# Kernel tuning notes

Measured on AMD Instinct MI355X. Metric: run time of the kernel, lower is better.

The kernel has to match this reference:

```python
import math
import jax, jax.numpy as jnp
import numpy as np

B, C, H, W = 8, 128, 128, 128

def _cosine_basis(n):
    pos = (jnp.arange(n, dtype=jnp.float32) + 0.5) / n          # [n]
    freq = jnp.arange(n, dtype=jnp.float32)[:, None]            # [n,1]
    basis = jnp.cos(freq * pos[None, :] * math.pi) * math.sqrt(2.0 / n)
    return basis.at[0, :].multiply(1.0 / math.sqrt(2.0))        # [n,n]


def setup_inputs() -> dict:
    key = jax.random.key(0)
    ks = jax.random.split(key, 12)
    s = 0.02
    return {
        "x":        jax.random.normal(ks[0], (B, C, H, W), jnp.float32),
        "dw_w":     jax.random.normal(ks[1], (C, 1, 3, 3), jnp.float32) * s,
        "dw_b":     jnp.zeros((C,), jnp.float32),
        "in_w":     jax.random.normal(ks[2], (2 * C, C), jnp.float32) * s,
        "in_b":     jnp.zeros((2 * C,), jnp.float32),
        "out_w":    jax.random.normal(ks[3], (C, C), jnp.float32) * s,
        "out_b":    jnp.zeros((C,), jnp.float32),
        "ln_w":     jnp.ones((C,), jnp.float32),
        "ln_b":     jnp.zeros((C,), jnp.float32),
        "ph_w":     jax.random.normal(ks[4], (C, C), jnp.float32) * s,
        "ph_b":     jnp.zeros((C,), jnp.float32),
        "wave_speed": jnp.ones((1,), jnp.float32),
        "damping":    jnp.full((1,), 0.1, jnp.float32),
        "freq_embed": jax.random.normal(ks[5], (H, W, C), jnp.float32) * s,
    }


def reference(x, dw_w, dw_b, in_w, in_b, out_w, out_b, ln_w, ln_b,
              ph_w, ph_b, wave_speed, damping, freq_embed):
    # depthwise 3x3 conv (groups=C), padding=1
    mixed = jax.lax.conv_general_dilated(
        x, dw_w, window_strides=(1, 1), padding=((1, 1), (1, 1)),
        dimension_numbers=("NCHW", "OIHW", "NCHW"), feature_group_count=C)
    mixed = mixed + dw_b[None, :, None, None]
    mixed = jnp.transpose(mixed, (0, 2, 3, 1))                  # [B,H,W,C]

    proj = mixed @ in_w.T + in_b                                # [B,H,W,2C]
    carrier, gate = jnp.split(proj, 2, axis=-1)

    cos_h = _cosine_basis(H)
    cos_w = _cosine_basis(W)
    # DCT-II along H then W
    spectral = jnp.einsum("bhwc,nh->bnwc", carrier, cos_h)
    spectral = jnp.einsum("bnwc,mw->bnmc", spectral, cos_w)     # [B,H,W,C] (freq)

    # phase modulation (base_resolution == H == W, so no resize)
    phase = jax.nn.gelu(freq_embed @ ph_w.T + ph_b, approximate=False)  # [H,W,C]
    wave_phase = wave_speed * phase                             # broadcast [H,W,C]
    vel_scale = jnp.sin(wave_phase) / jnp.maximum(jnp.abs(wave_speed), 1e-6)
    modulated = (jnp.cos(wave_phase) + vel_scale * (1.0 + 0.5 * damping)) * spectral

    # inverse DCT
    fused = jnp.einsum("bnmc,wm->bnwc", modulated, cos_w.T)
    fused = jnp.einsum("bnwc,hn->bhwc", fused, cos_h.T)         # [B,H,W,C]

    # LayerNorm over channels
    mu = jnp.mean(fused, axis=-1, keepdims=True)
    var = jnp.mean(jnp.square(fused - mu), axis=-1, keepdims=True)
    fused = (fused - mu) / jnp.sqrt(var + 1e-5) * ln_w + ln_b

    fused = fused * jax.nn.silu(gate)
    out = fused @ out_w.T + out_b                               # [B,H,W,C]
    return jnp.transpose(out, (0, 3, 1, 2))                     # [B,C,H,W]
```

## Files before the change

kernel.cpp:

```cpp
#include <hip/hip_runtime.h>
#include <math.h>

#ifndef M_PI
#define M_PI 3.14159265358979323846
#endif

typedef float fx4 __attribute__((ext_vector_type(4)));
typedef __bf16 bf16x8 __attribute__((ext_vector_type(8)));
typedef __bf16 bf16x4 __attribute__((ext_vector_type(4)));

__device__ __forceinline__ unsigned short f2bf(float f){
  union { float f; unsigned u; } v; v.f = f;
  unsigned r = v.u + 0x7FFFu + ((v.u >> 16) & 1u);
  return (unsigned short)(r >> 16);
}
__device__ __forceinline__ float bf2f(unsigned short u){
  union { unsigned u; float f; } v; v.u = ((unsigned)u) << 16;
  return v.f;
}
__device__ __forceinline__ int swz(int row, int colbyte){
  return row*256 + (colbyte ^ ((row & 7) << 4));
}

template<typename FA, typename FB>
__device__ __forceinline__ void run_gemm(FA la, FB lb, fx4 (&acc)[4][4]){
  bf16x8 a[2][4], b[2][4];
  #pragma unroll
  for (int mi=0;mi<4;mi++){ a[0][mi]=la(mi,0); b[0][mi]=lb(mi,0); }
  #pragma unroll
  for (int ks=0; ks<4; ks++){
    int cur = ks&1, nxt = cur^1;
    if (ks<3){
      #pragma unroll
      for (int mi=0;mi<4;mi++){ a[nxt][mi]=la(mi,ks+1); b[nxt][mi]=lb(mi,ks+1); }
    }
    #pragma unroll
    for (int mi=0;mi<4;mi++)
      #pragma unroll
      for (int ni=0;ni<4;ni++)
        acc[mi][ni] = __builtin_amdgcn_mfma_f32_16x16x32_bf16(a[cur][mi], b[cur][ni], acc[mi][ni], 0, 0, 0);
  }
}

__global__ __launch_bounds__(128) void prep_kernel(
    const float* __restrict__ in_w, const float* __restrict__ ph_w,
    const float* __restrict__ out_w,
    unsigned short* __restrict__ basis_bf, unsigned short* __restrict__ basisT_bf,
    unsigned short* __restrict__ ph_w_bf, unsigned short* __restrict__ in_w_bf,
    unsigned short* __restrict__ out_w_bf)
{
  int n = blockIdx.x;
  int h = threadIdx.x;
  double arg = (double)(n*(2*h+1)) * (M_PI/256.0);
  double v = cos(arg) * 0.125;
  if (n==0) v *= 0.7071067811865476;
  unsigned short bv = f2bf((float)v);
  basis_bf[n*128+h]  = bv;
  basisT_bf[h*128+n] = bv;
  ph_w_bf[n*128+h]  = f2bf(ph_w[n*128+h]);
  in_w_bf[n*128+h]        = f2bf(in_w[n*128+h]);
  in_w_bf[(n+128)*128+h]  = f2bf(in_w[(n+128)*128+h]);
  out_w_bf[n*128+h]       = f2bf(out_w[n*128+h]);
}

__global__ __launch_bounds__(256) void castfe_kernel(
  const float* __restrict__ fe, unsigned short* __restrict__ feb)
{
  int idx = blockIdx.x*256 + threadIdx.x;
  const float* s = fe + (size_t)idx*8;
  float4 f0 = *(const float4*)s;
  float4 f1 = *(const float4*)(s+4);
  unsigned short o[8];
  o[0]=f2bf(f0.x); o[1]=f2bf(f0.y); o[2]=f2bf(f0.z); o[3]=f2bf(f0.w);
  o[4]=f2bf(f1.x); o[5]=f2bf(f1.y); o[6]=f2bf(f1.z); o[7]=f2bf(f1.w);
  *(int4*)(feb + (size_t)idx*8) = *(const int4*)o;
}

__global__ __launch_bounds__(256) void projk_kernel(
  const unsigned short* __restrict__ feb, const unsigned short* __restrict__ ph_w_bf,
  float* __restrict__ projT)
{
  int r0 = blockIdx.x * 128;
  int t = threadIdx.x;
  int l = t & 63, wid = t >> 6;
  int wm = wid >> 1, wn = wid & 1;
  int lr = l & 15, lk = (l>>4)*8, ld4 = (l>>4)*4;
  fx4 acc[4][4];
  #pragma unroll
  for (int i=0;i<4;i++) for (int j=0;j<4;j++) acc[i][j] = (fx4){0.f,0.f,0.f,0.f};
  run_gemm(
    [&](int mi,int ks)->bf16x8{ return *(const bf16x8*)(feb + (size_t)(r0 + wm*64+mi*16+lr)*128 + ks*32+lk); },
    [&](int ni,int ks)->bf16x8{ return *(const bf16x8*)(ph_w_bf + (size_t)(wn*64+ni*16+lr)*128 + ks*32+lk); },
    acc);
  #pragma unroll
  for (int mi=0;mi<4;mi++)
    #pragma unroll
    for (int ni=0;ni<4;ni++){
      int c = wn*64 + ni*16 + lr;
      int r = r0 + wm*64 + mi*16 + ld4;
      *(fx4*)(projT + (size_t)c*16384 + r) = acc[mi][ni];
    }
}

__global__ __launch_bounds__(256) void modfin_kernel(
  const float* __restrict__ projT, const float* __restrict__ ph_b,
  const float* __restrict__ wave_speed, const float* __restrict__ damping,
  float* __restrict__ modT)
{
  int blk = blockIdx.x;
  int c = blk >> 4, qb = blk & 15;
  int t = threadIdx.x;
  int q = qb*8 + (t>>5);
  int p0 = (t & 31)*4;
  float ws0 = wave_speed[0];
  float dmp = damping[0];
  float inv = 1.0f / fmaxf(fabsf(ws0), 1e-6f);
  float dampf = 1.0f + 0.5f*dmp;
  float bc = ph_b[c];
  const float* src = projT + (size_t)c*16384 + q;
  float o[4];
  #pragma unroll
  for (int i=0;i<4;i++){
    float v = src[(size_t)(p0+i)*128] + bc;
    float g = 0.5f*v*(1.0f + erff(v*0.70710678118f));
    float wp = ws0*g;
    o[i] = __cosf(wp) + __sinf(wp)*inv*dampf;
  }
  *(float4*)(modT + ((size_t)c*128 + q)*128 + p0) = make_float4(o[0],o[1],o[2],o[3]);
}

__global__ __launch_bounds__(256) void dwconv_kernel(
  const float* __restrict__ x, const float* __restrict__ dw_w,
  const float* __restrict__ dw_b, unsigned short* __restrict__ conv)
{
  int blk = blockIdx.x;
  int plane = blk >> 2, band = blk & 3;
  int c = plane & 127;
  const float* xp = x + (size_t)plane*16384;
  unsigned short* op = conv + (size_t)plane*16384;
  const float* kw = dw_w + c*9;
  float k0=kw[0],k1=kw[1],k2=kw[2],k3=kw[3],k4=kw[4],k5=kw[5],k6=kw[6],k7=kw[7],k8=kw[8];
  float bias = dw_b[c];
  int t = threadIdx.x;
  int q = t & 31;
  int w0 = q*4;
  int rg = t >> 5;
  int h0 = band*32 + rg*4;
  bool le = (q==0), re = (q==31);

  float4 fA, fB, fC; float lA,rA,lB,rB,lC,rC;
  #define LOADROW(hh, f, l, r) { \
    int hc = (hh)<0 ? 0 : ((hh)>127 ? 127 : (hh)); \
    f = *(const float4*)(xp + hc*128 + w0); \
    float lu = __shfl_up(f.w, 1, 32); \
    float rd = __shfl_down(f.x, 1, 32); \
    l = le ? 0.f : lu; \
    r = re ? 0.f : rd; \
    if ((hh)<0 || (hh)>127){ f = make_float4(0.f,0.f,0.f,0.f); l=0.f; r=0.f; } \
  }
  LOADROW(h0-1, fA,lA,rA);
  LOADROW(h0,   fB,lB,rB);
  #pragma unroll
  for (int i=0;i<4;i++){
    LOADROW(h0+1+i, fC,lC,rC);
    float4 o;
    o.x = bias; o.y = bias; o.z = bias; o.w = bias;
    o.x = fmaf(k0,lA,  fmaf(k1,fA.x, fmaf(k2,fA.y, o.x)));
    o.y = fmaf(k0,fA.x,fmaf(k1,fA.y, fmaf(k2,fA.z, o.y)));
    o.z = fmaf(k0,fA.y,fmaf(k1,fA.z, fmaf(k2,fA.w, o.z)));
    o.w = fmaf(k0,fA.z,fmaf(k1,fA.w, fmaf(k2,rA,   o.w)));
    o.x = fmaf(k3,lB,  fmaf(k4,fB.x, fmaf(k5,fB.y, o.x)));
    o.y = fmaf(k3,fB.x,fmaf(k4,fB.y, fmaf(k5,fB.z, o.y)));
    o.z = fmaf(k3,fB.y,fmaf(k4,fB.z, fmaf(k5,fB.w, o.z)));
    o.w = fmaf(k3,fB.z,fmaf(k4,fB.w, fmaf(k5,rB,   o.w)));
    o.x = fmaf(k6,lC,  fmaf(k7,fC.x, fmaf(k8,fC.y, o.x)));
    o.y = fmaf(k6,fC.x,fmaf(k7,fC.y, fmaf(k8,fC.z, o.y)));
    o.z = fmaf(k6,fC.y,fmaf(k7,fC.z, fmaf(k8,fC.w, o.z)));
    o.w = fmaf(k6,fC.z,fmaf(k7,fC.w, fmaf(k8,rC,   o.w)));
    bf16x4 v;
    v[0]=(__bf16)o.x; v[1]=(__bf16)o.y; v[2]=(__bf16)o.z; v[3]=(__bf16)o.w;
    *(bf16x4*)(op + (size_t)(h0+i)*128 + w0) = v;
    fA=fB; lA=lB; rA=rB;
    fB=fC; lB=lC; rB=rC;
  }
  #undef LOADROW
}

__global__ __launch_bounds__(512) void inproj_kernel(
  const unsigned short* __restrict__ conv, const unsigned short* __restrict__ in_w_bf,
  const float* __restrict__ in_b, unsigned short* __restrict__ carrier,
  unsigned short* __restrict__ gate)
{
  __shared__ char A[32768];
  int blk = blockIdx.x; int b = blk>>7, h = blk&127;
  const unsigned short* C = conv + (size_t)b*2097152 + h*128;
  int t = threadIdx.x;
  {
    int wl = t & 63, grp = t >> 6;
    #pragma unroll
    for (int p=0;p<2;p++){
      int w = wl + 64*p;
      #pragma unroll
      for (int q=0;q<4;q++){
        int c0 = (q*8 + grp)*4;
        ushort4 v;
        v.x = C[(size_t)(c0+0)*16384 + w];
        v.y = C[(size_t)(c0+1)*16384 + w];
        v.z = C[(size_t)(c0+2)*16384 + w];
        v.w = C[(size_t)(c0+3)*16384 + w];
        *(ushort4*)(A + swz(w, c0*2)) = v;
      }
    }
  }
  __syncthreads();
  int l = t & 63, wid = t >> 6;
  int wm = wid >> 2, wn = wid & 3;
  int lr = l & 15, lk = (l>>4)*8, ld4 = (l>>4)*4;
  fx4 acc[4][4];
  #pragma unroll
  for (int i=0;i<4;i++) for (int j=0;j<4;j++) acc[i][j] = (fx4){0.f,0.f,0.f,0.f};
  run_gemm(
    [&](int mi,int ks)->bf16x8{ return *(const bf16x8*)(A + swz(wm*64+mi*16+lr, (ks*32+lk)*2)); },
    [&](int ni,int ks)->bf16x8{ return *(const bf16x8*)(in_w_bf + (size_t)(wn*64+ni*16+lr)*128 + ks*32+lk); },
    acc);
  __syncthreads();
  if (wn < 2){
    #pragma unroll
    for (int mi=0;mi<4;mi++)
      #pragma unroll
      for (int ni=0;ni<4;ni++){
        int n = wn*64 + ni*16 + lr;
        int w0 = wm*64 + mi*16 + ld4;
        float bias = in_b[n];
        ushort4 v;
        v.x=f2bf(acc[mi][ni][0]+bias); v.y=f2bf(acc[mi][ni][1]+bias);
        v.z=f2bf(acc[mi][ni][2]+bias); v.w=f2bf(acc[mi][ni][3]+bias);
        *(ushort4*)(carrier + (size_t)(b*128+n)*16384 + h*128 + w0) = v;
      }
  } else {
    #pragma unroll
    for (int mi=0;mi<4;mi++)
      #pragma unroll
      for (int ni=0;ni<4;ni++){
        int n = wn*64 + ni*16 + lr;
        int c = n - 128;
        int w0 = wm*64 + mi*16 + ld4;
        float bias = in_b[n];
        #pragma unroll
        for (int r=0;r<4;r++){
          float v = acc[mi][ni][r] + bias;
          float s = v / (1.0f + __expf(-v));
          *(unsigned short*)(A + swz(w0+r, c*2)) = f2bf(s);
        }
      }
  }
  __syncthreads();
  {
    unsigned short* gout = gate + (size_t)blk*16384;
    int w = t >> 2, cq = (t & 3) * 32;
    #pragma unroll
    for (int i=0;i<4;i++){
      int c0 = cq + i*8;
      int4 v = *(const int4*)(A + swz(w, c0*2));
      *(int4*)(gout + w*128 + c0) = v;
    }
  }
}

__global__ __launch_bounds__(256) void wave_kernel(
  const unsigned short* __restrict__ carrier,
  const unsigned short* __restrict__ basis,
  const unsigned short* __restrict__ basisT,
  const float* __restrict__ modT,
  unsigned short* __restrict__ fused)
{
  __shared__ char U[32768];
  int blk = blockIdx.x;
  int c = blk & 127;
  const unsigned short* X = carrier + (size_t)blk*16384;
  unsigned short* F = fused + (size_t)blk*16384;
  int t = threadIdx.x;
  int l = t & 63, wid = t >> 6;
  int wm = wid >> 1, wn = wid & 1;
  int lr = l & 15, lk = (l>>4)*8, ld4 = (l>>4)*4;
  fx4 acc[4][4];

  #pragma unroll
  for (int i=0;i<4;i++) for (int j=0;j<4;j++) acc[i][j] = (fx4){0.f,0.f,0.f,0.f};
  run_gemm(
    [&](int mi,int ks)->bf16x8{ return *(const bf16x8*)(X + (size_t)(wm*64+mi*16+lr)*128 + ks*32+lk); },
    [&](int ni,int ks)->bf16x8{ return *(const bf16x8*)(basis + (size_t)(wn*64+ni*16+lr)*128 + ks*32+lk); },
    acc);
  #pragma unroll
  for (int mi=0;mi<4;mi++)
    #pragma unroll
    for (int ni=0;ni<4;ni++){
      int m = wn*64 + ni*16 + lr, h0 = wm*64 + mi*16 + ld4;
      ushort4 v;
      v.x=f2bf(acc[mi][ni][0]); v.y=f2bf(acc[mi][ni][1]);
      v.z=f2bf(acc[mi][ni][2]); v.w=f2bf(acc[mi][ni][3]);
      *(ushort4*)(U + swz(m, h0*2)) = v;
    }
  __syncthreads();

  #pragma unroll
  for (int i=0;i<4;i++) for (int j=0;j<4;j++) acc[i][j] = (fx4){0.f,0.f,0.f,0.f};
  run_gemm(
    [&](int mi,int ks)->bf16x8{ return *(const bf16x8*)(basis + (size_t)(wm*64+mi*16+lr)*128 + ks*32+lk); },
    [&](int ni,int ks)->bf16x8{ return *(const bf16x8*)(U + swz(wn*64+ni*16+lr, (ks*32+lk)*2)); },
    acc);
  {
    const float* Mc = modT + (size_t)c*16384;
    #pragma unroll
    for (int mi=0;mi<4;mi++)
      #pragma unroll
      for (int ni=0;ni<4;ni++){
        int n0 = wm*64 + mi*16 + ld4, m = wn*64 + ni*16 + lr;
        fx4 mv = *(const fx4*)(Mc + (size_t)m*128 + n0);
        acc[mi][ni] *= mv;
      }
  }
  __syncthreads();
  #pragma unroll
  for (int mi=0;mi<4;mi++)
    #pragma unroll
    for (int ni=0;ni<4;ni++){
      int m = wn*64 + ni*16 + lr, n0 = wm*64 + mi*16 + ld4;
      ushort4 v;
      v.x=f2bf(acc[mi][ni][0]); v.y=f2bf(acc[mi][ni][1]);
      v.z=f2bf(acc[mi][ni][2]); v.w=f2bf(acc[mi][ni][3]);
      *(ushort4*)(U + swz(m, n0*2)) = v;
    }
  __syncthreads();

  #pragma unroll
  for (int i=0;i<4;i++) for (int j=0;j<4;j++) acc[i][j] = (fx4){0.f,0.f,0.f,0.f};
  run_gemm(
    [&](int mi,int ks)->bf16x8{ return *(const bf16x8*)(U + swz(wm*64+mi*16+lr, (ks*32+lk)*2)); },
    [&](int ni,int ks)->bf16x8{ return *(const bf16x8*)(basisT + (size_t)(wn*64+ni*16+lr)*128 + ks*32+lk); },
    acc);
  __syncthreads();
  #pragma unroll
  for (int mi=0;mi<4;mi++)
    #pragma unroll
    for (int ni=0;ni<4;ni++){
      int hh = wn*64 + ni*16 + lr, m0 = wm*64 + mi*16 + ld4;
      ushort4 v;
      v.x=f2bf(acc[mi][ni][0]); v.y=f2bf(acc[mi][ni][1]);
      v.z=f2bf(acc[mi][ni][2]); v.w=f2bf(acc[mi][ni][3]);
      *(ushort4*)(U + swz(hh, m0*2)) = v;
    }
  __syncthreads();

  #pragma unroll
  for (int i=0;i<4;i++) for (int j=0;j<4;j++) acc[i][j] = (fx4){0.f,0.f,0.f,0.f};
  run_gemm(
    [&](int mi,int ks)->bf16x8{ return *(const bf16x8*)(basisT + (size_t)(wm*64+mi*16+lr)*128 + ks*32+lk); },
    [&](int ni,int ks)->bf16x8{ return *(const bf16x8*)(U + swz(wn*64+ni*16+lr, (ks*32+lk)*2)); },
    acc);
  #pragma unroll
  for (int mi=0;mi<4;mi++)
    #pragma unroll
    for (int ni=0;ni<4;ni++){
      int hh = wn*64 + ni*16 + lr, w0 = wm*64 + mi*16 + ld4;
      ushort4 v;
      v.x=f2bf(acc[mi][ni][0]); v.y=f2bf(acc[mi][ni][1]);
      v.z=f2bf(acc[mi][ni][2]); v.w=f2bf(acc[mi][ni][3]);
      *(ushort4*)(F + hh*128 + w0) = v;
    }
}

__global__ __launch_bounds__(256) void final_kernel(
  const unsigned short* __restrict__ fused, const unsigned short* __restrict__ gate,
  const unsigned short* __restrict__ out_w_bf, const float* __restrict__ out_b,
  const float* __restrict__ ln_w, const float* __restrict__ ln_b,
  float* __restrict__ out)
{
  __shared__ char Fl[32768];
  __shared__ char Al[32768];
  __shared__ float red[256], red2[256];
  __shared__ float mu[128], rs[128];
  int blk = blockIdx.x; int b = blk>>7, h = blk&127;
  const unsigned short* Fsrc = fused + (size_t)b*2097152 + h*128;
  const unsigned short* G = gate + (size_t)blk*16384;
  int t = threadIdx.x;
  {
    int c = t>>1, wq = (t&1)*64;
    #pragma unroll
    for (int i=0;i<8;i++){
      int w0 = wq + i*8;
      int4 v = *(const int4*)(Fsrc + (size_t)c*16384 + w0);
      *(int4*)(Fl + swz(c, w0*2)) = v;
    }
  }
  __syncthreads();
  {
    int w = t&127, half = t>>7;
    float s=0.f, q=0.f;
    for (int i=0;i<64;i++){
      int c = half*64 + i;
      float f = bf2f(*(const unsigned short*)(Fl + swz(c, w*2)));
      s += f; q = fmaf(f,f,q);
    }
    red[t]=s; red2[t]=q;
  }
  __syncthreads();
  if (t < 128){
    float ss = red[t]+red[t+128], qq = red2[t]+red2[t+128];
    float m = ss*(1.f/128.f);
    float var = qq*(1.f/128.f) - m*m;
    mu[t]=m; rs[t]=rsqrtf(var+1e-5f);
  }
  __syncthreads();
  {
    int w = t>>1, cq = (t&1)*64;
    float m_ = mu[w], r_ = rs[w];
    #pragma unroll
    for (int i=0;i<8;i++){
      int c0 = cq + i*8;
      ushort4 g0 = *(const ushort4*)(G + (size_t)w*128 + c0);
      ushort4 g1 = *(const ushort4*)(G + (size_t)w*128 + c0 + 4);
      unsigned short ov[8];
      unsigned short gv[8] = {g0.x,g0.y,g0.z,g0.w,g1.x,g1.y,g1.z,g1.w};
      #pragma unroll
      for (int j=0;j<8;j++){
        int cc = c0+j;
        float f = bf2f(*(const unsigned short*)(Fl + swz(cc, w*2)));
        float a = fmaf((f-m_)*r_, ln_w[cc], ln_b[cc]) * bf2f(gv[j]);
        ov[j] = f2bf(a);
      }
      *(int4*)(Al + swz(w, c0*2)) = *(const int4*)ov;
    }
  }
  __syncthreads();
  int l = t & 63, wid = t >> 6;
  int wm = wid >> 1, wn = wid & 1;
  int lr = l & 15, lk = (l>>4)*8, ld4 = (l>>4)*4;
  fx4 acc[4][4];
  #pragma unroll
  for (int i=0;i<4;i++) for (int j=0;j<4;j++) acc[i][j] = (fx4){0.f,0.f,0.f,0.f};
  run_gemm(
    [&](int mi,int ks)->bf16x8{ return *(const bf16x8*)(Al + swz(wm*64+mi*16+lr, (ks*32+lk)*2)); },
    [&](int ni,int ks)->bf16x8{ return *(const bf16x8*)(out_w_bf + (size_t)(wn*64+ni*16+lr)*128 + ks*32+lk); },
    acc);
  #pragma unroll
  for (int mi=0;mi<4;mi++)
    #pragma unroll
    for (int ni=0;ni<4;ni++){
      int j = wn*64 + ni*16 + lr, w0 = wm*64 + mi*16 + ld4;
      float bj = out_b[j];
      fx4 o = acc[mi][ni];
      o[0]+=bj; o[1]+=bj; o[2]+=bj; o[3]+=bj;
      *(fx4*)(out + ((size_t)(b*128 + j)*128 + h)*128 + w0) = o;
    }
}

extern "C" void kernel_launch(void* const* d_in, const int* in_sizes, int n_in,
                              void* d_out, int out_size, void* d_ws, size_t ws_size,
                              hipStream_t stream)
{
  const float* x      = (const float*)d_in[0];
  const float* dw_w   = (const float*)d_in[1];
  const float* dw_b   = (const float*)d_in[2];
  const float* in_w   = (const float*)d_in[3];
  const float* in_b   = (const float*)d_in[4];
  const float* out_w  = (const float*)d_in[5];
  const float* out_b  = (const float*)d_in[6];
  const float* ln_w   = (const float*)d_in[7];
  const float* ln_b   = (const float*)d_in[8];
  const float* ph_w   = (const float*)d_in[9];
  const float* ph_b   = (const float*)d_in[10];
  const float* wsp    = (const float*)d_in[11];
  const float* dmp    = (const float*)d_in[12];
  const float* fe     = (const float*)d_in[13];
  float* outp = (float*)d_out;

  float* modT  = (float*)d_ws;
  float* projT = modT + 2097152;
  unsigned short* feb      = (unsigned short*)(projT + 2097152);
  unsigned short* conv     = feb     + 2097152;
  unsigned short* carrier  = conv    + 16777216;
  unsigned short* gate     = carrier + 16777216;
  unsigned short* fusedb   = gate    + 16777216;
  unsigned short* basis_bf = fusedb  + 16777216;
  unsigned short* basisT_bf= basis_bf + 16384;
  unsigned short* in_w_bf  = basisT_bf + 16384;
  unsigned short* out_w_bf = in_w_bf + 32768;
  unsigned short* ph_w_bf  = out_w_bf + 16384;

  prep_kernel<<<128,128,0,stream>>>(in_w, ph_w, out_w, basis_bf, basisT_bf, ph_w_bf, in_w_bf, out_w_bf);
  castfe_kernel<<<1024,256,0,stream>>>(fe, feb);
  projk_kernel<<<128,256,0,stream>>>(feb, ph_w_bf, projT);
  modfin_kernel<<<2048,256,0,stream>>>(projT, ph_b, wsp, dmp, modT);
  dwconv_kernel<<<4096,256,0,stream>>>(x, dw_w, dw_b, conv);
  inproj_kernel<<<1024,512,0,stream>>>(conv, in_w_bf, in_b, carrier, gate);
  wave_kernel<<<1024,256,0,stream>>>(carrier, basis_bf, basisT_bf, modT, fusedb);
  final_kernel<<<1024,256,0,stream>>>(fusedb, gate, out_w_bf, out_b, ln_w, ln_b, outp);
}
```

Baseline: 183.2 us.

## Process two batch slices per wave_kernel block to share DCT basis and mod loads

Each wave_kernel block now handles two (b,c) slices, blk and blk+512, which share the same channel c. Basis fragments and modulation factors are loaded once and applied to both slices, and the MFMA streams are interleaved. The grid is halved to 512 blocks and shared memory doubles to 64KB, with roughly twice the accumulator registers per thread. This cuts per-slice global traffic and adds independent MFMA work to hide latency, at the risk of lower occupancy or register spills. bf16 conversion also moves from the manual rounding helper to native __bf16 casts.

```diff
diff --git a/kernel.cpp b/kernel.cpp
--- a/kernel.cpp
+++ b/kernel.cpp
@@ -39,6 +39,52 @@
       #pragma unroll
       for (int ni=0;ni<4;ni++)
         acc[mi][ni] = __builtin_amdgcn_mfma_f32_16x16x32_bf16(a[cur][mi], b[cur][ni], acc[mi][ni], 0, 0, 0);
+  }
+}
+
+template<typename FA0, typename FA1, typename FB>
+__device__ __forceinline__ void run_pair_sharedB(FA0 la0, FA1 la1, FB lb,
+                                                 fx4 (&acc0)[4][4], fx4 (&acc1)[4][4]){
+  bf16x8 a0[2][4], a1[2][4], b[2][4];
+  #pragma unroll
+  for (int mi=0;mi<4;mi++){ a0[0][mi]=la0(mi,0); a1[0][mi]=la1(mi,0); b[0][mi]=lb(mi,0); }
+  #pragma unroll
+  for (int ks=0; ks<4; ks++){
+    int cur = ks&1, nxt = cur^1;
+    if (ks<3){
+      #pragma unroll
+      for (int mi=0;mi<4;mi++){ a0[nxt][mi]=la0(mi,ks+1); a1[nxt][mi]=la1(mi,ks+1); b[nxt][mi]=lb(mi,ks+1); }
+    }
+    #pragma unroll
+    for (int mi=0;mi<4;mi++)
+      #pragma unroll
+      for (int ni=0;ni<4;ni++){
+        acc0[mi][ni] = __builtin_amdgcn_mfma_f32_16x16x32_bf16(a0[cur][mi], b[cur][ni], acc0[mi][ni], 0, 0, 0);
+        acc1[mi][ni] = __builtin_amdgcn_mfma_f32_16x16x32_bf16(a1[cur][mi], b[cur][ni], acc1[mi][ni], 0, 0, 0);
+      }
+  }
+}
+
+template<typename FA, typename FB0, typename FB1>
+__device__ __forceinline__ void run_pair_sharedA(FA la, FB0 lb0, FB1 lb1,
+                                                 fx4 (&acc0)[4][4], fx4 (&acc1)[4][4]){
+  bf16x8 a[2][4], b0[2][4], b1[2][4];
+  #pragma unroll
+  for (int mi=0;mi<4;mi++){ a[0][mi]=la(mi,0); b0[0][mi]=lb0(mi,0); b1[0][mi]=lb1(mi,0); }
+  #pragma unroll
+  for (int ks=0; ks<4; ks++){
+    int cur = ks&1, nxt = cur^1;
+    if (ks<3){
+      #pragma unroll
+      for (int mi=0;mi<4;mi++){ a[nxt][mi]=la(mi,ks+1); b0[nxt][mi]=lb0(mi,ks+1); b1[nxt][mi]=lb1(mi,ks+1); }
+    }
+    #pragma unroll
+    for (int mi=0;mi<4;mi++)
+      #pragma unroll
+      for (int ni=0;ni<4;ni++){
+        acc0[mi][ni] = __builtin_amdgcn_mfma_f32_16x16x32_bf16(a[cur][mi], b0[cur][ni], acc0[mi][ni], 0, 0, 0);
+        acc1[mi][ni] = __builtin_amdgcn_mfma_f32_16x16x32_bf16(a[cur][mi], b1[cur][ni], acc1[mi][ni], 0, 0, 0);
+      }
   }
 }
 
@@ -274,41 +320,49 @@
   const float* __restrict__ modT,
   unsigned short* __restrict__ fused)
 {
-  __shared__ char U[32768];
+  __shared__ char U0[32768];
+  __shared__ char U1[32768];
   int blk = blockIdx.x;
   int c = blk & 127;
-  const unsigned short* X = carrier + (size_t)blk*16384;
-  unsigned short* F = fused + (size_t)blk*16384;
+  const unsigned short* X0 = carrier + (size_t)blk*16384;
+  const unsigned short* X1 = carrier + (size_t)(blk+512)*16384;
+  unsigned short* F0 = fused + (size_t)blk*16384;
+  unsigned short* F1 = fused + (size_t)(blk+512)*16384;
   int t = threadIdx.x;
   int l = t & 63, wid = t >> 6;
   int wm = wid >> 1, wn = wid & 1;
   int lr = l & 15, lk = (l>>4)*8, ld4 = (l>>4)*4;
-  fx4 acc[4][4];
-
-  #pragma unroll
-  for (int i=0;i<4;i++) for (int j=0;j<4;j++) acc[i][j] = (fx4){0.f,0.f,0.f,0.f};
-  run_gemm(
-    [&](int mi,int ks)->bf16x8{ return *(const bf16x8*)(X + (size_t)(wm*64+mi*16+lr)*128 + ks*32+lk); },
+  fx4 acc0[4][4], acc1[4][4];
+
+  #define ZACC { _Pragma("unroll") for (int i=0;i<4;i++) _Pragma("unroll") for (int j=0;j<4;j++){ acc0[i][j]=(fx4){0.f,0.f,0.f,0.f}; acc1[i][j]=(fx4){0.f,0.f,0.f,0.f}; } }
+  #define TSTORE(BUF0, BUF1, ROW, COL) { \
+    _Pragma("unroll") for (int mi=0;mi<4;mi++) \
+      _Pragma("unroll") for (int ni=0;ni<4;ni++){ \
+        int rr = wn*64 + ni*16 + lr, cc = wm*64 + mi*16 + ld4; (void)rr; (void)cc; \
+        bf16x4 v0, v1; \
+        v0[0]=(__bf16)acc0[mi][ni][0]; v0[1]=(__bf16)acc0[mi][ni][1]; \
+        v0[2]=(__bf16)acc0[mi][ni][2]; v0[3]=(__bf16)acc0[mi][ni][3]; \
+        v1[0]=(__bf16)acc1[mi][ni][0]; v1[1]=(__bf16)acc1[mi][ni][1]; \
+        v1[2]=(__bf16)acc1[mi][ni][2]; v1[3]=(__bf16)acc1[mi][ni][3]; \
+        *(bf16x4*)(BUF0 + swz(rr, cc*2)) = v0; \
+        *(bf16x4*)(BUF1 + swz(rr, cc*2)) = v1; \
+      } }
+
+  ZACC;
+  run_pair_sharedB(
+    [&](int mi,int ks)->bf16x8{ return *(const bf16x8*)(X0 + (size_t)(wm*64+mi*16+lr)*128 + ks*32+lk); },
+    [&](int mi,int ks)->bf16x8{ return *(const bf16x8*)(X1 + (size_t)(wm*64+mi*16+lr)*128 + ks*32+lk); },
     [&](int ni,int ks)->bf16x8{ return *(const bf16x8*)(basis + (size_t)(wn*64+ni*16+lr)*128 + ks*32+lk); },
-    acc);
-  #pragma unroll
-  for (int mi=0;mi<4;mi++)
-    #pragma unroll
-    for (int ni=0;ni<4;ni++){
-      int m = wn*64 + ni*16 + lr, h0 = wm*64 + mi*16 + ld4;
-      ushort4 v;
-      v.x=f2bf(acc[mi][ni][0]); v.y=f2bf(acc[mi][ni][1]);
-      v.z=f2bf(acc[mi][ni][2]); v.w=f2bf(acc[mi][ni][3]);
-      *(ushort4*)(U + swz(m, h0*2)) = v;
-    }
-  __syncthreads();
-
-  #pragma unroll
-  for (int i=0;i<4;i++) for (int j=0;j<4;j++) acc[i][j] = (fx4){0.f,0.f,0.f,0.f};
-  run_gemm(
+    acc0, acc1);
+  TSTORE(U0, U1, m, h);
+  __syncthreads();
+
+  ZACC;
+  run_pair_sharedA(
     [&](int mi,int ks)->bf16x8{ return *(const bf16x8*)(basis + (size_t)(wm*64+mi*16+lr)*128 + ks*32+lk); },
-    [&](int ni,int ks)->bf16x8{ return *(const bf16x8*)(U + swz(wn*64+ni*16+lr, (ks*32+lk)*2)); },
-    acc);
+    [&](int ni,int ks)->bf16x8{ return *(const bf16x8*)(U0 + swz(wn*64+ni*16+lr, (ks*32+lk)*2)); },
+    [&](int ni,int ks)->bf16x8{ return *(const bf16x8*)(U1 + swz(wn*64+ni*16+lr, (ks*32+lk)*2)); },
+    acc0, acc1);
   {
     const float* Mc = modT + (size_t)c*16384;
     #pragma unroll
@@ -317,57 +371,45 @@
       for (int ni=0;ni<4;ni++){
         int n0 = wm*64 + mi*16 + ld4, m = wn*64 + ni*16 + lr;
         fx4 mv = *(const fx4*)(Mc + (size_t)m*128 + n0);
-        acc[mi][ni] *= mv;
-      }
-  }
-  __syncthreads();
-  #pragma unroll
-  for (int mi=0;mi<4;mi++)
-    #pragma unroll
-    for (int ni=0;ni<4;ni++){
-      int m = wn*64 + ni*16 + lr, n0 = wm*64 + mi*16 + ld4;
-      ushort4 v;
-      v.x=f2bf(acc[mi][ni][0]); v.y=f2bf(acc[mi][ni][1]);
-      v.z=f2bf(acc[mi][ni][2]); v.w=f2bf(acc[mi][ni][3]);
-      *(ushort4*)(U + swz(m, n0*2)) = v;
-    }
-  __syncthreads();
-
-  #pragma unroll
-  for (int i=0;i<4;i++) for (int j=0;j<4;j++) acc[i][j] = (fx4){0.f,0.f,0.f,0.f};
-  run_gemm(
-    [&](int mi,int ks)->bf16x8{ return *(const bf16x8*)(U + swz(wm*64+mi*16+lr, (ks*32+lk)*2)); },
+        acc0[mi][ni] *= mv;
+        acc1[mi][ni] *= mv;
+      }
+  }
+  __syncthreads();
+  TSTORE(U0, U1, m, n);
+  __syncthreads();
+
+  ZACC;
+  run_pair_sharedB(
+    [&](int mi,int ks)->bf16x8{ return *(const bf16x8*)(U0 + swz(wm*64+mi*16+lr, (ks*32+lk)*2)); },
+    [&](int mi,int ks)->bf16x8{ return *(const bf16x8*)(U1 + swz(wm*64+mi*16+lr, (ks*32+lk)*2)); },
     [&](int ni,int ks)->bf16x8{ return *(const bf16x8*)(basisT + (size_t)(wn*64+ni*16+lr)*128 + ks*32+lk); },
-    acc);
-  __syncthreads();
-  #pragma unroll
-  for (int mi=0;mi<4;mi++)
-    #pragma unroll
-    for (int ni=0;ni<4;ni++){
-      int hh = wn*64 + ni*16 + lr, m0 = wm*64 + mi*16 + ld4;
-      ushort4 v;
-      v.x=f2bf(acc[mi][ni][0]); v.y=f2bf(acc[mi][ni][1]);
-      v.z=f2bf(acc[mi][ni][2]); v.w=f2bf(acc[mi][ni][3]);
-      *(ushort4*)(U + swz(hh, m0*2)) = v;
-    }
-  __syncthreads();
-
-  #pragma unroll
-  for (int i=0;i<4;i++) for (int j=0;j<4;j++) acc[i][j] = (fx4){0.f,0.f,0.f,0.f};
-  run_gemm(
+    acc0, acc1);
+  __syncthreads();
+  TSTORE(U0, U1, h, m);
+  __syncthreads();
+
+  ZACC;
+  run_pair_sharedA(
     [&](int mi,int ks)->bf16x8{ return *(const bf16x8*)(basisT + (size_t)(wm*64+mi*16+lr)*128 + ks*32+lk); },
-    [&](int ni,int ks)->bf16x8{ return *(const bf16x8*)(U + swz(wn*64+ni*16+lr, (ks*32+lk)*2)); },
-    acc);
+    [&](int ni,int ks)->bf16x8{ return *(const bf16x8*)(U0 + swz(wn*64+ni*16+lr, (ks*32+lk)*2)); },
+    [&](int ni,int ks)->bf16x8{ return *(const bf16x8*)(U1 + swz(wn*64+ni*16+lr, (ks*32+lk)*2)); },
+    acc0, acc1);
   #pragma unroll
   for (int mi=0;mi<4;mi++)
     #pragma unroll
     for (int ni=0;ni<4;ni++){
       int hh = wn*64 + ni*16 + lr, w0 = wm*64 + mi*16 + ld4;
-      ushort4 v;
-      v.x=f2bf(acc[mi][ni][0]); v.y=f2bf(acc[mi][ni][1]);
-      v.z=f2bf(acc[mi][ni][2]); v.w=f2bf(acc[mi][ni][3]);
-      *(ushort4*)(F + hh*128 + w0) = v;
-    }
+      bf16x4 v0, v1;
+      v0[0]=(__bf16)acc0[mi][ni][0]; v0[1]=(__bf16)acc0[mi][ni][1];
+      v0[2]=(__bf16)acc0[mi][ni][2]; v0[3]=(__bf16)acc0[mi][ni][3];
+      v1[0]=(__bf16)acc1[mi][ni][0]; v1[1]=(__bf16)acc1[mi][ni][1];
+      v1[2]=(__bf16)acc1[mi][ni][2]; v1[3]=(__bf16)acc1[mi][ni][3];
+      *(bf16x4*)(F0 + hh*128 + w0) = v0;
+      *(bf16x4*)(F1 + hh*128 + w0) = v1;
+    }
+  #undef ZACC
+  #undef TSTORE
 }
 
 __global__ __launch_bounds__(256) void final_kernel(
@@ -494,6 +536,6 @@
   modfin_kernel<<<2048,256,0,stream>>>(projT, ph_b, wsp, dmp, modT);
   dwconv_kernel<<<4096,256,0,stream>>>(x, dw_w, dw_b, conv);
   inproj_kernel<<<1024,512,0,stream>>>(conv, in_w_bf, in_b, carrier, gate);
-  wave_kernel<<<1024,256,0,stream>>>(carrier, basis_bf, basisT_bf, modT, fusedb);
+  wave_kernel<<<512,256,0,stream>>>(carrier, basis_bf, basisT_bf, modT, fusedb);
   final_kernel<<<1024,256,0,stream>>>(fusedb, gate, out_w_bf, out_b, ln_w, ln_b, outp);
 }
```

Result: faster. 171.9 us (-6.2%).
